# Kernel optimization log

Hardware: AMD Instinct MI355X
Metric: run time of the kernel (lower is better)

Reference implementation:

```python
import jax, jax.numpy as jnp
import numpy as np

AFWD = 0.999
ABKW = 0.99
EPS = 1e-5
B, C, H, W = 32, 256, 64, 64


def lin_momentum(prev, curr, stream, momentum):
    # Batch-parallel EMA via sliding-window weighted sums (conv1d-with-powers trick).
    b = curr.shape[0]
    pow_vec = momentum ** jnp.arange(b - 1, -1, -1, dtype=curr.dtype)  # [b]
    seq = jnp.concatenate([prev[1:], curr], axis=0)  # [2b-1, C]
    idx = jnp.arange(b)[:, None] + jnp.arange(b)[None, :]  # [b, b] window indices
    tmp = jnp.einsum('j,ijc->ic', pow_vec, seq[idx])  # [b, C]
    new = (momentum ** b) * stream + (1.0 - momentum) * tmp
    stale = jnp.concatenate([stream[-1:], new[:-1]], axis=0)  # shifted (stale) stream for fprop
    return stale, new


def cn_forward(x, m, var, m_p, var_p):
    mu = x.mean((2, 3))  # [b, C] per-sample per-channel mean
    v = ((x - mu[:, :, None, None]) ** 2).mean((2, 3))  # [b, C] variance
    _mu_b, mu_b = lin_momentum(m_p, mu, m, AFWD)
    var_current = v + AFWD * (mu - _mu_b) ** 2
    _var_b, var_b = lin_momentum(var_p, var_current, var, AFWD)
    scale = jnp.sqrt(_var_b + EPS)[:, :, None, None]
    out = (x - _mu_b[:, :, None, None]) / scale
    return out, scale


def setup_inputs():
    key = jax.random.key(0)
    return {
        'x': jax.random.normal(key, (B, C, H, W), dtype=jnp.float32),
        'm': jnp.zeros((B, C), jnp.float32),
        'var': jnp.ones((B, C), jnp.float32),
        'm_p': jnp.zeros((B, C), jnp.float32),
        'var_p': jnp.ones((B, C), jnp.float32),
        'u': jnp.zeros((B, C), jnp.float32),
        'u_p': jnp.zeros((B, C), jnp.float32),
        'v_p': jnp.zeros((B, C), jnp.float32),
        'beta_p': jnp.zeros((B, C), jnp.float32),
        'alpha_p': jnp.ones((B, C), jnp.float32),
    }


def reference(x, m, var, m_p, var_p, u, u_p, v_p, beta_p, alpha_p):
    # u/u_p/v_p/beta_p/alpha_p are backward-pass control buffers; unused in fprop.
    out, _ = cn_forward(x, m, var, m_p, var_p)
    return out
```

## Files before the change

### kernel.cpp

```cpp
#include <hip/hip_runtime.h>

#define NB 32
#define NC 256
#define HW 4096
#define AFWD 0.999f
#define EPS 1e-5f
#define CH 4
#define NCHUNK (NB / CH)

typedef float f32x4 __attribute__((ext_vector_type(4)));

__device__ __forceinline__ void ema_chunk(
    int k, int l,
    float& run_munew, float& run_varnew,
    float* seq, float* seq2,
    const float* e_m, const float* e_var, const float* e_powv,
    float (*sp)[4][2], float* s_must, float* s_rs)
{
    const float one_m = 1.f - AFWD;
    const float pw    = e_powv[l & 31];
    const float mB32  = e_powv[NB];
#pragma unroll
    for (int ii = 0; ii < CH; ++ii) {
        const int i = k * CH + ii;
        float S  = sp[ii][0][0] + sp[ii][1][0] + sp[ii][2][0] + sp[ii][3][0];
        float SS = sp[ii][0][1] + sp[ii][1][1] + sp[ii][2][1] + sp[ii][3][1];
        float mu_i = S * (1.f / HW);
        float v_i  = SS * (1.f / HW) - mu_i * mu_i;
        if (l == 0) seq[NB - 1 + i] = mu_i;
        float dot = pw * seq[i + (l & 31)];
#pragma unroll
        for (int o = 1; o < 32; o <<= 1) dot += __shfl_xor(dot, o, 64);
        float munew = mB32 * e_m[i] + one_m * dot;
        float must  = i ? run_munew : e_m[NB - 1];
        float d  = mu_i - must;
        float vc = v_i + AFWD * d * d;
        if (l == 0) seq2[NB - 1 + i] = vc;
        float dot2 = pw * seq2[i + (l & 31)];
#pragma unroll
        for (int o = 1; o < 32; o <<= 1) dot2 += __shfl_xor(dot2, o, 64);
        float varnew = mB32 * e_var[i] + one_m * dot2;
        float varst  = i ? run_varnew : e_var[NB - 1];
        run_munew  = munew;
        run_varnew = varnew;
        if (l == 0) {
            s_must[i] = must;
            s_rs[i]   = 1.f / sqrtf(varst + EPS);
        }
    }
}

__global__ __launch_bounds__(1024) void cn_pipe(
    const float* __restrict__ x,
    const float* __restrict__ m,
    const float* __restrict__ var,
    const float* __restrict__ m_p,
    const float* __restrict__ var_p,
    float* __restrict__ out)
{
    const int c = blockIdx.x;
    const int t = threadIdx.x;
    const int w = t >> 6, l = t & 63;
    const int p = w >> 2;
    const int q = w & 3;

    __shared__ float seq[2 * NB - 1], seq2[2 * NB - 1];
    __shared__ float e_m[NB], e_var[NB];
    __shared__ float e_powv[NB + 1];
    __shared__ float s_must[NB], s_rs[NB];
    __shared__ float sp[CH][4][2];

    if (t < NB - 1) {
        seq[t]  = m_p[(t + 1) * NC + c];
        seq2[t] = var_p[(t + 1) * NC + c];
    }
    if (t < NB) {
        e_m[t]   = m[t * NC + c];
        e_var[t] = var[t * NC + c];
    }
    if (t == 0) {
        float pw = 1.f;
        for (int j = NB - 1; j >= 0; --j) { e_powv[j] = pw; pw *= AFWD; }
        e_powv[NB] = pw;
    }

    float run_munew = 0.f, run_varnew = 0.f;
    f32x4 dA[4], dB[4];

#define LOADC(DST, K) do {                                                    \
        const int b_ = (K) * CH + p;                                          \
        const f32x4* xp_ = (const f32x4*)(x + ((size_t)b_ * NC + c) * HW);    \
        _Pragma("unroll")                                                     \
        for (int i_ = 0; i_ < 4; ++i_) DST[i_] = xp_[q * 256 + i_ * 64 + l];  \
    } while (0)

#define CHUNKB(K, CUR, NXT) do {                                              \
        if ((K) + 1 < NCHUNK) LOADC(NXT, (K) + 1);         \
        float s_ = 0.f, ss_ = 0.f;                                            \
        _Pragma("unroll")                                                     \
        for (int i_ = 0; i_ < 4; ++i_) {                                      \
            f32x4 a_ = CUR[i_];                                               \
            s_  += a_.x + a_.y + a_.z + a_.w;                                 \
            ss_ += a_.x * a_.x + a_.y * a_.y + a_.z * a_.z + a_.w * a_.w;     \
        }                                                                     \
        _Pragma("unroll")                                                     \
        for (int o_ = 32; o_ > 0; o_ >>= 1) {                                 \
            s_  += __shfl_down(s_, o_, 64);                                   \
            ss_ += __shfl_down(ss_, o_, 64);                                  \
        }                                                                     \
        if (l == 0) { sp[p][q][0] = s_; sp[p][q][1] = ss_; }                  \
        __syncthreads();                                                      \
        if (w == 0)                                                           \
            ema_chunk((K), l, run_munew, run_varnew, seq, seq2,               \
                      e_m, e_var, e_powv, sp, s_must, s_rs);                  \
        __syncthreads();                                                      \
        {                                                                     \
            const int b_ = (K) * CH + p;                                      \
            const float mu_ = s_must[b_], rs_ = s_rs[b_];                     \
            f32x4* op_ = (f32x4*)(out + ((size_t)b_ * NC + c) * HW);          \
            _Pragma("unroll")                                                 \
            for (int i_ = 0; i_ < 4; ++i_)                                    \
                __builtin_nontemporal_store((CUR[i_] - mu_) * rs_,            \
                                            &op_[q * 256 + i_ * 64 + l]);     \
        }                                                                     \
    } while (0)

    LOADC(dA, 0);
    CHUNKB(0, dA, dB);
    CHUNKB(1, dB, dA);
    CHUNKB(2, dA, dB);
    CHUNKB(3, dB, dA);
    CHUNKB(4, dA, dB);
    CHUNKB(5, dB, dA);
    CHUNKB(6, dA, dB);
    CHUNKB(7, dB, dA);

#undef LOADC
#undef CHUNKB
}

extern "C" void kernel_launch(void* const* d_in, const int* in_sizes, int n_in,
                              void* d_out, int out_size, void* d_ws, size_t ws_size,
                              hipStream_t stream) {
    const float* x     = (const float*)d_in[0];
    const float* m     = (const float*)d_in[1];
    const float* var   = (const float*)d_in[2];
    const float* m_p   = (const float*)d_in[3];
    const float* var_p = (const float*)d_in[4];
    float* out = (float*)d_out;

    cn_pipe<<<NC, 1024, 0, stream>>>(x, m, var, m_p, var_p, out);
}
```

Baseline: 45.73 us.

## Replace serialized wave-0 EMA with redundant per-thread sliding recurrence, drop barrier

```diff
diff --git a/kernel.cpp b/kernel.cpp
--- a/kernel.cpp
+++ b/kernel.cpp
@@ -9,46 +9,6 @@
 #define NCHUNK (NB / CH)
 
 typedef float f32x4 __attribute__((ext_vector_type(4)));
-
-__device__ __forceinline__ void ema_chunk(
-    int k, int l,
-    float& run_munew, float& run_varnew,
-    float* seq, float* seq2,
-    const float* e_m, const float* e_var, const float* e_powv,
-    float (*sp)[4][2], float* s_must, float* s_rs)
-{
-    const float one_m = 1.f - AFWD;
-    const float pw    = e_powv[l & 31];
-    const float mB32  = e_powv[NB];
-#pragma unroll
-    for (int ii = 0; ii < CH; ++ii) {
-        const int i = k * CH + ii;
-        float S  = sp[ii][0][0] + sp[ii][1][0] + sp[ii][2][0] + sp[ii][3][0];
-        float SS = sp[ii][0][1] + sp[ii][1][1] + sp[ii][2][1] + sp[ii][3][1];
-        float mu_i = S * (1.f / HW);
-        float v_i  = SS * (1.f / HW) - mu_i * mu_i;
-        if (l == 0) seq[NB - 1 + i] = mu_i;
-        float dot = pw * seq[i + (l & 31)];
-#pragma unroll
-        for (int o = 1; o < 32; o <<= 1) dot += __shfl_xor(dot, o, 64);
-        float munew = mB32 * e_m[i] + one_m * dot;
-        float must  = i ? run_munew : e_m[NB - 1];
-        float d  = mu_i - must;
-        float vc = v_i + AFWD * d * d;
-        if (l == 0) seq2[NB - 1 + i] = vc;
-        float dot2 = pw * seq2[i + (l & 31)];
-#pragma unroll
-        for (int o = 1; o < 32; o <<= 1) dot2 += __shfl_xor(dot2, o, 64);
-        float varnew = mB32 * e_var[i] + one_m * dot2;
-        float varst  = i ? run_varnew : e_var[NB - 1];
-        run_munew  = munew;
-        run_varnew = varnew;
-        if (l == 0) {
-            s_must[i] = must;
-            s_rs[i]   = 1.f / sqrtf(varst + EPS);
-        }
-    }
-}
 
 __global__ __launch_bounds__(1024) void cn_pipe(
     const float* __restrict__ x,
@@ -64,27 +24,34 @@
     const int p = w >> 2;
     const int q = w & 3;
 
-    __shared__ float seq[2 * NB - 1], seq2[2 * NB - 1];
-    __shared__ float e_m[NB], e_var[NB];
-    __shared__ float e_powv[NB + 1];
-    __shared__ float s_must[NB], s_rs[NB];
-    __shared__ float sp[CH][4][2];
+    __shared__ float m_s[NB], var_s[NB], mp_s[NB], vp_s[NB];
+    __shared__ float sp[2][CH][4][2];
 
-    if (t < NB - 1) {
-        seq[t]  = m_p[(t + 1) * NC + c];
-        seq2[t] = var_p[(t + 1) * NC + c];
-    }
-    if (t < NB) {
-        e_m[t]   = m[t * NC + c];
-        e_var[t] = var[t * NC + c];
-    }
-    if (t == 0) {
-        float pw = 1.f;
-        for (int j = NB - 1; j >= 0; --j) { e_powv[j] = pw; pw *= AFWD; }
-        e_powv[NB] = pw;
+    if (t < NB) { m_s[t] = m[t * NC + c]; var_s[t] = var[t * NC + c]; }
+    if (t >= 1 && t < NB) {
+        mp_s[t] = m_p[t * NC + c];
+        vp_s[t] = var_p[t * NC + c];
     }
 
-    float run_munew = 0.f, run_varnew = 0.f;
+    float D = 0.f, D2 = 0.f;
+    if (l < NB - 1) {
+        float pw = 1.f;
+        for (int k = l; k < NB - 1; ++k) pw *= AFWD;
+        D  = pw * m_p[(l + 1) * NC + c];
+        D2 = pw * var_p[(l + 1) * NC + c];
+    }
+#pragma unroll
+    for (int o = 1; o < 64; o <<= 1) {
+        D  += __shfl_xor(D, o, 64);
+        D2 += __shfl_xor(D2, o, 64);
+    }
+
+    float a32 = 1.f;
+#pragma unroll
+    for (int k = 0; k < NB; ++k) a32 *= AFWD;
+    const float one_m = 1.f - AFWD;
+
+    float tmp = 0.f, tmp2 = 0.f, prev_munew = 0.f, prev_varnew = 0.f;
     f32x4 dA[4], dB[4];
 
 #define LOADC(DST, K) do {                                                    \
@@ -108,19 +75,37 @@
             s_  += __shfl_down(s_, o_, 64);                                   \
             ss_ += __shfl_down(ss_, o_, 64);                                  \
         }                                                                     \
-        if (l == 0) { sp[p][q][0] = s_; sp[p][q][1] = ss_; }                  \
+        if (l == 0) { sp[(K) & 1][p][q][0] = s_; sp[(K) & 1][p][q][1] = ss_; }\
         __syncthreads();                                                      \
-        if (w == 0)                                                           \
-            ema_chunk((K), l, run_munew, run_varnew, seq, seq2,               \
-                      e_m, e_var, e_powv, sp, s_must, s_rs);                  \
-        __syncthreads();                                                      \
+        float muP = 0.f, rsP = 1.f;                                           \
+        _Pragma("unroll")                                                     \
+        for (int ii = 0; ii < CH; ++ii) {                                     \
+            const int i = (K) * CH + ii;                                      \
+            float S_  = sp[(K) & 1][ii][0][0] + sp[(K) & 1][ii][1][0]         \
+                      + sp[(K) & 1][ii][2][0] + sp[(K) & 1][ii][3][0];        \
+            float SS_ = sp[(K) & 1][ii][0][1] + sp[(K) & 1][ii][1][1]         \
+                      + sp[(K) & 1][ii][2][1] + sp[(K) & 1][ii][3][1];        \
+            float mu_i = S_ * (1.f / HW);                                     \
+            float v_i  = SS_ * (1.f / HW) - mu_i * mu_i;                      \
+            if (i == 0) tmp = D + mu_i;                                       \
+            else        tmp = AFWD * tmp - a32 * mp_s[i] + mu_i;              \
+            float munew = a32 * m_s[i] + one_m * tmp;                         \
+            float must  = (i == 0) ? m_s[NB - 1] : prev_munew;                \
+            float d_ = mu_i - must;                                           \
+            float vc = v_i + AFWD * d_ * d_;                                  \
+            if (i == 0) tmp2 = D2 + vc;                                       \
+            else        tmp2 = AFWD * tmp2 - a32 * vp_s[i] + vc;              \
+            float varnew = a32 * var_s[i] + one_m * tmp2;                     \
+            float varst  = (i == 0) ? var_s[NB - 1] : prev_varnew;            \
+            prev_munew = munew; prev_varnew = varnew;                         \
+            if (ii == p) { muP = must; rsP = 1.f / sqrtf(varst + EPS); }      \
+        }                                                                     \
         {                                                                     \
             const int b_ = (K) * CH + p;                                      \
-            const float mu_ = s_must[b_], rs_ = s_rs[b_];                     \
             f32x4* op_ = (f32x4*)(out + ((size_t)b_ * NC + c) * HW);          \
             _Pragma("unroll")                                                 \
             for (int i_ = 0; i_ < 4; ++i_)                                    \
-                __builtin_nontemporal_store((CUR[i_] - mu_) * rs_,            \
+                __builtin_nontemporal_store((CUR[i_] - muP) * rsP,            \
                                             &op_[q * 256 + i_ * 64 + l]);     \
         }                                                                     \
     } while (0)
```

Result: faster. 44.60 us (-2.5%).
